# Performance work log

Measured on AMD Instinct MI355X. Metric: run time of the kernel, lower is better.

Reference implementation:

```python
import jax, jax.numpy as jnp
import numpy as np

EMBED_DIM = 1024
NUM_HEADS = 16
HEAD_DIM = EMBED_DIM // NUM_HEADS
SCALE = HEAD_DIM ** -0.5
B, S = 2, 2048


def setup_inputs() -> dict:
    key = jax.random.key(0)
    ks = jax.random.split(key, 11)
    lim = 1.0 / np.sqrt(EMBED_DIM)
    def lin(kw, kb):
        W = jax.random.uniform(kw, (EMBED_DIM, EMBED_DIM), jnp.float32, -lim, lim)
        b = jax.random.uniform(kb, (EMBED_DIM,), jnp.float32, -lim, lim)
        return W, b
    Wq, bq = lin(ks[0], ks[1])
    Wk, bk = lin(ks[2], ks[3])
    Wv, bv = lin(ks[4], ks[5])
    Wo, bo = lin(ks[6], ks[7])
    query = jax.random.normal(ks[8], (B, S, EMBED_DIM), jnp.float32)
    key_t = jax.random.normal(ks[9], (B, S, EMBED_DIM), jnp.float32)
    value = jax.random.normal(ks[10], (B, S, EMBED_DIM), jnp.float32)
    return {"query": query, "key": key_t, "value": value,
            "Wq": Wq, "bq": bq, "Wk": Wk, "bk": bk,
            "Wv": Wv, "bv": bv, "Wo": Wo, "bo": bo}


def reference(query, key, value, Wq, bq, Wk, bk, Wv, bv, Wo, bo):
    # 'flash' path with attn_mask=None == full softmax attention (chunking is
    # only an execution schedule; per-chunk softmax is over the full key axis).
    b, s, _ = query.shape
    def heads(x, W, bias):
        y = x @ W.T + bias                      # [b, s, E]
        return y.reshape(b, s, NUM_HEADS, HEAD_DIM).transpose(0, 2, 1, 3)  # [b, h, s, d]
    q = heads(query, Wq, bq)
    k = heads(key, Wk, bk)
    v = heads(value, Wv, bv)
    scores = jnp.einsum('bhqd,bhkd->bhqk', q, k) * SCALE
    attn = jax.nn.softmax(scores, axis=-1)
    out = jnp.einsum('bhqk,bhkd->bhqd', attn, v)
    out = out.transpose(0, 2, 1, 3).reshape(b, s, EMBED_DIM)
    return out @ Wo.T + bo
```

## Files before the change

kernel.cpp:

```cpp
#include <hip/hip_runtime.h>

typedef unsigned short u16;
typedef unsigned int u32;
typedef __attribute__((ext_vector_type(8))) __bf16 bf16x8;
typedef __attribute__((ext_vector_type(4))) float f32x4;
typedef __attribute__((ext_vector_type(4))) unsigned short u16x4;
typedef __attribute__((ext_vector_type(8))) unsigned short u16x8;
typedef __attribute__((ext_vector_type(2))) unsigned int u32x2;
typedef __attribute__((ext_vector_type(4))) unsigned int u32x4;

#define DEV static __device__ __forceinline__

DEV void async_copy16(const void* g, void* l) {
  __builtin_amdgcn_global_load_lds((const __attribute__((address_space(1))) void*)g,
                                   (__attribute__((address_space(3))) void*)l, 16, 0, 0);
}
DEV float b2f(u16 s) { union { unsigned u; float f; } v; v.u = ((unsigned)s) << 16; return v.f; }
DEV u16 f2b(float f) {
  union { float f; unsigned u; } v; v.f = f;
  unsigned r = v.u + 0x7FFFu + ((v.u >> 16) & 1u);
  return (u16)(r >> 16);
}
DEV u32 pack2bf(float a, float b) {
  u32 ua = __float_as_uint(a) + 0x8000u;
  u32 ub = __float_as_uint(b) + 0x8000u;
  return __builtin_amdgcn_perm(ub, ua, 0x07060302u);
}

#define MFMA(a, b, c) __builtin_amdgcn_mfma_f32_16x16x32_bf16((a), (b), (c), 0, 0, 0)

__global__ void detect_dtype(const unsigned* __restrict__ q, int* __restrict__ flag) {
  const int lane = threadIdx.x;
  const unsigned w = q[lane];
  const unsigned e = (w >> 7) & 0xFFu;
  const bool inr = (e >= 100u && e <= 132u);
  const unsigned long long m = __ballot(inr);
  if (lane == 0) flag[0] = (__popcll(m) >= 48) ? 1 : 0;
}

__global__ void convert_inputs(
    const void* s0, const void* s1, const void* s2,
    const void* s3, const void* s4, const void* s5, const void* s6,
    const void* s7, const void* s8, const void* s9, const void* s10,
    u16* __restrict__ d0, u16* __restrict__ d1, u16* __restrict__ d2,
    u16* __restrict__ d3, u16* __restrict__ d4, u16* __restrict__ d5, u16* __restrict__ d6,
    float* __restrict__ e7, float* __restrict__ e8, float* __restrict__ e9, float* __restrict__ e10,
    const int* __restrict__ flag)
{
  const int bi = blockIdx.y;
  const void* src = nullptr; u16* db = nullptr; float* df = nullptr; int n = 0;
  switch (bi) {
    case 0:  src = s0;  db = d0; n = 4194304; break;
    case 1:  src = s1;  db = d1; n = 4194304; break;
    case 2:  src = s2;  db = d2; n = 4194304; break;
    case 3:  src = s3;  db = d3; n = 1048576; break;
    case 4:  src = s4;  db = d4; n = 1048576; break;
    case 5:  src = s5;  db = d5; n = 1048576; break;
    case 6:  src = s6;  db = d6; n = 1048576; break;
    case 7:  src = s7;  df = e7; n = 1024; break;
    case 8:  src = s8;  df = e8; n = 1024; break;
    case 9:  src = s9;  df = e9; n = 1024; break;
    default: src = s10; df = e10; n = 1024; break;
  }
  const int isbf = flag[0];
  const int stride = gridDim.x * 256 * 8;
  for (int i = (blockIdx.x * 256 + threadIdx.x) * 8; i < n; i += stride) {
    if (db) {
      u16x8 v;
      if (isbf) {
        v = *(const u16x8*)((const u16*)src + i);
      } else {
        const float* sf = (const float*)src;
#pragma unroll
        for (int j = 0; j < 8; ++j) v[j] = f2b(sf[i + j]);
      }
      *(u16x8*)(db + i) = v;
    } else {
#pragma unroll
      for (int j = 0; j < 8; ++j) {
        float x = isbf ? b2f(((const u16*)src)[i + j]) : ((const float*)src)[i + j];
        df[i + j] = x;
      }
    }
  }
}

__global__ void gemm_qkv(const u16* __restrict__ X0, const u16* __restrict__ X1, const u16* __restrict__ X2,
                         const u16* __restrict__ W0, const u16* __restrict__ W1, const u16* __restrict__ W2,
                         const float* __restrict__ B0, const float* __restrict__ B1, const float* __restrict__ B2,
                         u16* __restrict__ Y0, u16* __restrict__ Y1, u16* __restrict__ Y2,
                         float* __restrict__ Yf, const int* __restrict__ flag, int mode0)
{
  __shared__ __align__(16) u16 smem[17408];

  const int z = blockIdx.z;
  const u16* X  = (z == 0) ? X0 : ((z == 1) ? X1 : X2);
  const u16* W  = (z == 0) ? W0 : ((z == 1) ? W1 : W2);
  const float* Bi = (z == 0) ? B0 : ((z == 1) ? B1 : B2);
  u16* Y        = (z == 0) ? Y0 : ((z == 1) ? Y1 : Y2);
  const int mode = mode0 ? mode0 : z;
  const int outbf = flag[0];

  const int t = threadIdx.x, wave = t >> 6, lane = t & 63;
  const int lane15 = lane & 15, quad = lane >> 4;

  const int L = blockIdx.y * 8 + blockIdx.x;
  const int wrk = (L & 7) * 32 + (L >> 3);
  const int m0 = (wrk >> 3) * 128, n0 = (wrk & 7) * 128;

  const u16* gA = X + (size_t)(m0 + wave * 16 + (lane >> 2)) * 1024 + (lane & 3) * 8;
  const u16* gB = W + (size_t)(n0 + wave * 16 + (lane >> 2)) * 1024 + (lane & 3) * 8;

  f32x4 acc[4][4];
#pragma unroll
  for (int i = 0; i < 4; ++i)
#pragma unroll
    for (int j = 0; j < 4; ++j) acc[i][j] = (f32x4){0.f, 0.f, 0.f, 0.f};

  const int wr = wave >> 1, wc = wave & 1;

  u16* lA0 = smem + wave * 512;
  u16* lB0 = smem + 4096 + wave * 512;
  u16* lA1 = smem + 8192 + wave * 512;
  u16* lB1 = smem + 12288 + wave * 512;

  auto stage = [&](u16* lA, u16* lB) {
    async_copy16(gA, lA);
    async_copy16(gA + 64 * 1024, lA + 64 * 32);
    async_copy16(gB, lB);
    async_copy16(gB + 64 * 1024, lB + 64 * 32);
    gA += 32; gB += 32;
  };
  auto compute = [&](const u16* As_, const u16* Bs_) {
    bf16x8 af[4], bfv[4];
#pragma unroll
    for (int mt = 0; mt < 4; ++mt)
      af[mt] = *(const bf16x8*)&As_[(wr * 64 + mt * 16 + lane15) * 32 + quad * 8];
#pragma unroll
    for (int nt = 0; nt < 4; ++nt)
      bfv[nt] = *(const bf16x8*)&Bs_[(wc * 64 + nt * 16 + lane15) * 32 + quad * 8];
    __builtin_amdgcn_s_setprio(1);
#pragma unroll
    for (int mt = 0; mt < 4; ++mt)
#pragma unroll
      for (int nt = 0; nt < 4; ++nt)
        acc[mt][nt] = MFMA(af[mt], bfv[nt], acc[mt][nt]);
    __builtin_amdgcn_s_setprio(0);
  };

  stage(lA0, lB0);
  __syncthreads();

  for (int k0 = 0; k0 < 1024; k0 += 64) {
    if (k0 + 32 < 1024) stage(lA1, lB1);
    compute(smem, smem + 4096);
    __syncthreads();
    if (k0 + 64 < 1024) stage(lA0, lB0);
    compute(smem + 8192, smem + 12288);
    __syncthreads();
  }

  const float qscale = 0.125f * 1.44269504088896340736f;

  if (mode == 2) {
    u16* T2 = smem;
#pragma unroll
    for (int mt = 0; mt < 4; ++mt) {
      const int sl_base = wr * 64 + mt * 16 + quad * 4;
#pragma unroll
      for (int nt = 0; nt < 4; ++nt) {
        const int nn = wc * 64 + nt * 16 + lane15;
        const float bias_v = Bi[n0 + nn];
#pragma unroll
        for (int r = 0; r < 4; ++r) {
          const int sl = sl_base + r;
          T2[nn * 136 + sl] = f2b(acc[mt][nt][r] + bias_v);
        }
      }
    }
    __syncthreads();
    const size_t grow0 = (size_t)(m0 >> 11) * 1024 + n0;
    const int col0 = m0 & 2047;
#pragma unroll
    for (int i = 0; i < 8; ++i) {
      const int id = i * 256 + t;
      const int row = id >> 4, ch = id & 15;
      *(u16x8*)&Y[(grow0 + row) * 2048 + col0 + ch * 8] = *(const u16x8*)&T2[row * 136 + ch * 8];
    }
    return;
  }

#pragma unroll
  for (int mt = 0; mt < 4; ++mt) {
    const int m_base = m0 + wr * 64 + mt * 16 + quad * 4;
#pragma unroll
    for (int nt = 0; nt < 4; ++nt) {
      const int n = n0 + wc * 64 + nt * 16 + lane15;
      const float bias_v = Bi[n];
#pragma unroll
      for (int r = 0; r < 4; ++r) {
        const int m = m_base + r;
        float v = acc[mt][nt][r] + bias_v;
        if (mode == 0) v *= qscale;
        if (mode == 3) {
          if (outbf) Y[(size_t)m * 1024 + n] = f2b(v);
          else       Yf[(size_t)m * 1024 + n] = v;
        } else {
          size_t addr = (((size_t)(m >> 11) * 16 + (n >> 6)) * 2048 + (size_t)(m & 2047)) * 64 + (n & 63);
          Y[addr] = f2b(v);
        }
      }
    }
  }
}

__global__ __launch_bounds__(256, 4) void flash_attn(const u16* __restrict__ Qs, const u16* __restrict__ Ks,
                                                     const u16* __restrict__ Vt, u16* __restrict__ AO)
{
  __shared__ __align__(16) u16 smem[16384];
  u16* Kt = smem;
  u16* Vs = smem + 8192;

  const int t = threadIdx.x, wave = t >> 6, lane = t & 63;
  const int lane15 = lane & 15, quad = lane >> 4;
  const int l7 = lane15 & 7;
  const int h = wave >> 1;
  const int c = wave & 1;

  const int Lb = blockIdx.y * 16 + blockIdx.x;
  const int wrk = (Lb & 7) * 128 + (Lb >> 3);
  const int bh = wrk >> 5;
  const int q0 = (wrk & 31) * 64;

  const u16* Qb = Qs + ((size_t)bh * 2048 + q0) * 64;
  const u16* Kb = Ks + (size_t)bh * 2048 * 64;
  const u16* Vb = Vt + (size_t)bh * 64 * 2048;

  const int krow = lane >> 3;
  const int kchunk = (lane & 7) ^ (krow & 7);
  const int vrow = lane >> 4;
  const int vchunk = (lane & 15) ^ (((wave & 1) << 2) + vrow);

#pragma unroll
  for (int r = 0; r < 2; ++r)
    async_copy16(Qb + (size_t)(r * 32 + wave * 8 + krow) * 64 + kchunk * 8,
                 &Kt[(r * 32 + wave * 8) * 64]);
  __syncthreads();
  bf16x8 aq[2][2];
#pragma unroll
  for (int mt = 0; mt < 2; ++mt)
#pragma unroll
    for (int ks = 0; ks < 2; ++ks)
      aq[mt][ks] = *(const bf16x8*)&Kt[(h * 32 + mt * 16 + lane15) * 64 + ((ks * 4 + quad) ^ l7) * 8];
  __syncthreads();

  f32x4 acc_o[2][4];
  f32x4 acc_l[2];
#pragma unroll
  for (int mt = 0; mt < 2; ++mt) {
    acc_l[mt] = (f32x4){0.f, 0.f, 0.f, 0.f};
#pragma unroll
    for (int i = 0; i < 4; ++i) acc_o[mt][i] = (f32x4){0.f, 0.f, 0.f, 0.f};
  }

  u16x8 ou;
#pragma unroll
  for (int j = 0; j < 8; ++j) ou[j] = 0x3F80;
  const bf16x8 ones = __builtin_bit_cast(bf16x8, ou);

  for (int kt = 0; kt < 16; ++kt) {
#pragma unroll
    for (int r = 0; r < 4; ++r)
      async_copy16(Kb + (size_t)(kt * 128 + r * 32 + wave * 8 + krow) * 64 + kchunk * 8,
                   &Kt[(r * 32 + wave * 8) * 64]);
#pragma unroll
    for (int r = 0; r < 4; ++r)
      async_copy16(Vb + (size_t)(r * 16 + wave * 4 + vrow) * 2048 + kt * 128 + vchunk * 8,
                   &Vs[(r * 16 + wave * 4) * 128]);
    __syncthreads();

#pragma unroll
    for (int g = 0; g < 2; ++g) {
      const int ks2 = c * 2 + g;
      bf16x8 bk[2][2];
#pragma unroll
      for (int no = 0; no < 2; ++no)
#pragma unroll
        for (int ks = 0; ks < 2; ++ks)
          bk[no][ks] = *(const bf16x8*)&Kt[(c * 64 + g * 32 + no * 16 + lane15) * 64 + ((ks * 4 + quad) ^ l7) * 8];

      bf16x8 pa[2];
#pragma unroll
      for (int mt = 0; mt < 2; ++mt) {
        f32x4 s2[2];
        s2[0] = (f32x4){0.f, 0.f, 0.f, 0.f};
        s2[1] = (f32x4){0.f, 0.f, 0.f, 0.f};
        __builtin_amdgcn_s_setprio(1);
#pragma unroll
        for (int no = 0; no < 2; ++no)
#pragma unroll
          for (int ks = 0; ks < 2; ++ks)
            s2[no] = MFMA(bk[no][ks], aq[mt][ks], s2[no]);
        __builtin_amdgcn_s_setprio(0);

        float e0[4], e1[4];
#pragma unroll
        for (int rg = 0; rg < 4; ++rg) {
          e0[rg] = __builtin_amdgcn_exp2f(s2[0][rg]);
          e1[rg] = __builtin_amdgcn_exp2f(s2[1][rg]);
        }
        const u32 x0 = pack2bf(e0[0], e0[1]), x1 = pack2bf(e0[2], e0[3]);
        const u32 y0 = pack2bf(e1[0], e1[1]), y1 = pack2bf(e1[2], e1[3]);
        const u32x2 rA = __builtin_amdgcn_permlane32_swap(x0, y0, false, false);
        const u32x2 rB = __builtin_amdgcn_permlane32_swap(x1, y1, false, false);
        const u32x2 f0 = __builtin_amdgcn_permlane16_swap(rA[0], rA[1], false, false);
        const u32x2 f1 = __builtin_amdgcn_permlane16_swap(rB[0], rB[1], false, false);
        const u32x4 paw = (u32x4){f0[0], f1[0], f0[1], f1[1]};
        pa[mt] = __builtin_bit_cast(bf16x8, paw);
      }

      bf16x8 bv[4];
#pragma unroll
      for (int dt = 0; dt < 4; ++dt)
        bv[dt] = *(const bf16x8*)&Vs[(dt * 16 + lane15) * 128 + ((ks2 * 4 + quad) ^ l7) * 8];
      __builtin_amdgcn_s_setprio(1);
#pragma unroll
      for (int mt = 0; mt < 2; ++mt) {
#pragma unroll
        for (int dt = 0; dt < 4; ++dt)
          acc_o[mt][dt] = MFMA(pa[mt], bv[dt], acc_o[mt][dt]);
        acc_l[mt] = MFMA(pa[mt], ones, acc_l[mt]);
      }
      __builtin_amdgcn_s_setprio(0);
    }
    __syncthreads();
  }

  float* Of = (float*)smem;
  if (c == 1) {
#pragma unroll
    for (int mt = 0; mt < 2; ++mt)
#pragma unroll
      for (int dt = 0; dt < 4; ++dt)
#pragma unroll
        for (int rg = 0; rg < 4; ++rg)
          Of[h * 2048 + (mt * 16 + quad * 4 + rg) * 64 + dt * 16 + lane15] = acc_o[mt][dt][rg];
  }
  __syncthreads();
  if (c == 0) {
#pragma unroll
    for (int mt = 0; mt < 2; ++mt)
#pragma unroll
      for (int dt = 0; dt < 4; ++dt)
#pragma unroll
        for (int rg = 0; rg < 4; ++rg)
          acc_o[mt][dt][rg] += Of[h * 2048 + (mt * 16 + quad * 4 + rg) * 64 + dt * 16 + lane15];
  }
  __syncthreads();
  float* Lf = (float*)smem;
  if (c == 1 && lane15 == 0) {
#pragma unroll
    for (int mt = 0; mt < 2; ++mt)
#pragma unroll
      for (int rg = 0; rg < 4; ++rg)
        Lf[h * 32 + mt * 16 + quad * 4 + rg] = acc_l[mt][rg];
  }
  __syncthreads();
  float rinv[2][4];
  if (c == 0) {
#pragma unroll
    for (int mt = 0; mt < 2; ++mt)
#pragma unroll
      for (int rg = 0; rg < 4; ++rg)
        rinv[mt][rg] = 1.0f / (acc_l[mt][rg] + Lf[h * 32 + mt * 16 + quad * 4 + rg]);
  }
  __syncthreads();

  u16* T = smem;
  if (c == 0) {
#pragma unroll
    for (int mt = 0; mt < 2; ++mt)
#pragma unroll
      for (int dt = 0; dt < 4; ++dt)
#pragma unroll
        for (int rg = 0; rg < 4; ++rg)
          T[(h * 32 + mt * 16 + quad * 4 + rg) * 72 + dt * 16 + lane15] =
              f2b(acc_o[mt][dt][rg] * rinv[mt][rg]);
  }
  __syncthreads();

  const int b = bh >> 4, hh = bh & 15;
#pragma unroll
  for (int i = 0; i < 2; ++i) {
    const int id = i * 256 + t;
    const int row = id >> 3, ch = id & 7;
    *(u16x8*)&AO[((size_t)b * 2048 + q0 + row) * 1024 + hh * 64 + ch * 8] =
        *(const u16x8*)&T[row * 72 + ch * 8];
  }
}

extern "C" void kernel_launch(void* const* d_in, const int* in_sizes, int n_in,
                              void* d_out, int out_size, void* d_ws, size_t ws_size,
                              hipStream_t stream)
{
  const void* query = d_in[0];
  const void* key_  = d_in[1];
  const void* value = d_in[2];
  const void* Wq = d_in[3]; const void* bq = d_in[4];
  const void* Wk = d_in[5]; const void* bk = d_in[6];
  const void* Wv = d_in[7]; const void* bv = d_in[8];
  const void* Wo = d_in[9]; const void* bo = d_in[10];

  u16* ws = (u16*)d_ws;
  u16* Qs  = ws;
  u16* Ks  = Qs + 4194304;
  u16* Vt  = Ks + 4194304;
  u16* AO  = Vt + 4194304;
  u16* Xq  = AO + 4194304;
  u16* Xk  = Xq + 4194304;
  u16* Xv  = Xk + 4194304;
  u16* Wqc = Xv + 4194304;
  u16* Wkc = Wqc + 1048576;
  u16* Wvc = Wkc + 1048576;
  u16* Woc = Wvc + 1048576;
  float* Bc = (float*)(Woc + 1048576);
  int* flag = (int*)(Bc + 4096);

  detect_dtype<<<1, 64, 0, stream>>>((const unsigned*)query, flag);
  convert_inputs<<<dim3(128, 11), 256, 0, stream>>>(
      query, key_, value, Wq, Wk, Wv, Wo, bq, bk, bv, bo,
      Xq, Xk, Xv, Wqc, Wkc, Wvc, Woc,
      Bc, Bc + 1024, Bc + 2048, Bc + 3072, flag);

  gemm_qkv<<<dim3(8, 32, 3), 256, 0, stream>>>(Xq, Xk, Xv, Wqc, Wkc, Wvc,
                                               Bc, Bc + 1024, Bc + 2048,
                                               Qs, Ks, Vt, nullptr, flag, 0);
  flash_attn<<<dim3(16, 64), 256, 0, stream>>>(Qs, Ks, Vt, AO);
  gemm_qkv<<<dim3(8, 32, 1), 256, 0, stream>>>(AO, AO, AO, Woc, Woc, Woc,
                                               Bc + 3072, Bc + 3072, Bc + 3072,
                                               (u16*)d_out, (u16*)d_out, (u16*)d_out,
                                               (float*)d_out, flag, 3);
}
```

Before: 218.9 us.

## Double-buffer K/V tiles in flash attention to overlap loads with compute

Doubles the flash-attention shared-memory buffer so the K and V tiles for the next key block are fetched asynchronously while the current block is being computed. The loop is unrolled by two and alternates between the two halves, leaving a single barrier per tile instead of a load-then-barrier pattern that left compute waiting on memory. The cost is twice the LDS per block, and the launch-bounds occupancy hint drops from 4 to 2 blocks, so fewer waves are resident to hide latency.

```diff
diff --git a/kernel.cpp b/kernel.cpp
--- a/kernel.cpp
+++ b/kernel.cpp
@@ -214,12 +214,10 @@
   }
 }
 
-__global__ __launch_bounds__(256, 4) void flash_attn(const u16* __restrict__ Qs, const u16* __restrict__ Ks,
+__global__ __launch_bounds__(256, 2) void flash_attn(const u16* __restrict__ Qs, const u16* __restrict__ Ks,
                                                      const u16* __restrict__ Vt, u16* __restrict__ AO)
 {
-  __shared__ __align__(16) u16 smem[16384];
-  u16* Kt = smem;
-  u16* Vs = smem + 8192;
+  __shared__ __align__(16) u16 smem[32768];
 
   const int t = threadIdx.x, wave = t >> 6, lane = t & 63;
   const int lane15 = lane & 15, quad = lane >> 4;
@@ -241,17 +239,30 @@
   const int vrow = lane >> 4;
   const int vchunk = (lane & 15) ^ (((wave & 1) << 2) + vrow);
 
+  auto stage = [&](int kt, u16* buf) {
+    u16* Ktb = buf;
+    u16* Vsb = buf + 8192;
+#pragma unroll
+    for (int r = 0; r < 4; ++r)
+      async_copy16(Kb + (size_t)(kt * 128 + r * 32 + wave * 8 + krow) * 64 + kchunk * 8,
+                   &Ktb[(r * 32 + wave * 8) * 64]);
+#pragma unroll
+    for (int r = 0; r < 4; ++r)
+      async_copy16(Vb + (size_t)(r * 16 + wave * 4 + vrow) * 2048 + kt * 128 + vchunk * 8,
+                   &Vsb[(r * 16 + wave * 4) * 128]);
+  };
+
 #pragma unroll
   for (int r = 0; r < 2; ++r)
     async_copy16(Qb + (size_t)(r * 32 + wave * 8 + krow) * 64 + kchunk * 8,
-                 &Kt[(r * 32 + wave * 8) * 64]);
+                 &smem[(r * 32 + wave * 8) * 64]);
   __syncthreads();
   bf16x8 aq[2][2];
 #pragma unroll
   for (int mt = 0; mt < 2; ++mt)
 #pragma unroll
     for (int ks = 0; ks < 2; ++ks)
-      aq[mt][ks] = *(const bf16x8*)&Kt[(h * 32 + mt * 16 + lane15) * 64 + ((ks * 4 + quad) ^ l7) * 8];
+      aq[mt][ks] = *(const bf16x8*)&smem[(h * 32 + mt * 16 + lane15) * 64 + ((ks * 4 + quad) ^ l7) * 8];
   __syncthreads();
 
   f32x4 acc_o[2][4];
@@ -268,17 +279,9 @@
   for (int j = 0; j < 8; ++j) ou[j] = 0x3F80;
   const bf16x8 ones = __builtin_bit_cast(bf16x8, ou);
 
-  for (int kt = 0; kt < 16; ++kt) {
-#pragma unroll
-    for (int r = 0; r < 4; ++r)
-      async_copy16(Kb + (size_t)(kt * 128 + r * 32 + wave * 8 + krow) * 64 + kchunk * 8,
-                   &Kt[(r * 32 + wave * 8) * 64]);
-#pragma unroll
-    for (int r = 0; r < 4; ++r)
-      async_copy16(Vb + (size_t)(r * 16 + wave * 4 + vrow) * 2048 + kt * 128 + vchunk * 8,
-                   &Vs[(r * 16 + wave * 4) * 128]);
-    __syncthreads();
-
+  auto compute = [&](const u16* buf) {
+    const u16* Ktb = buf;
+    const u16* Vsb = buf + 8192;
 #pragma unroll
     for (int g = 0; g < 2; ++g) {
       const int ks2 = c * 2 + g;
@@ -287,7 +290,7 @@
       for (int no = 0; no < 2; ++no)
 #pragma unroll
         for (int ks = 0; ks < 2; ++ks)
-          bk[no][ks] = *(const bf16x8*)&Kt[(c * 64 + g * 32 + no * 16 + lane15) * 64 + ((ks * 4 + quad) ^ l7) * 8];
+          bk[no][ks] = *(const bf16x8*)&Ktb[(c * 64 + g * 32 + no * 16 + lane15) * 64 + ((ks * 4 + quad) ^ l7) * 8];
 
       bf16x8 pa[2];
 #pragma unroll
@@ -322,7 +325,7 @@
       bf16x8 bv[4];
 #pragma unroll
       for (int dt = 0; dt < 4; ++dt)
-        bv[dt] = *(const bf16x8*)&Vs[(dt * 16 + lane15) * 128 + ((ks2 * 4 + quad) ^ l7) * 8];
+        bv[dt] = *(const bf16x8*)&Vsb[(dt * 16 + lane15) * 128 + ((ks2 * 4 + quad) ^ l7) * 8];
       __builtin_amdgcn_s_setprio(1);
 #pragma unroll
       for (int mt = 0; mt < 2; ++mt) {
@@ -333,6 +336,17 @@
       }
       __builtin_amdgcn_s_setprio(0);
     }
+  };
+
+  stage(0, smem);
+  __syncthreads();
+
+  for (int kt = 0; kt < 16; kt += 2) {
+    if (kt + 1 < 16) stage(kt + 1, smem + 16384);
+    compute(smem);
+    __syncthreads();
+    if (kt + 2 < 16) stage(kt + 2, smem);
+    compute(smem + 16384);
     __syncthreads();
   }
 
```

New measurement: 226.5 us. 3.5% more time.
